# Kernel tuning notes

Hardware: AMD Instinct MI355X
Metric: run time of the kernel (lower is better)

Reference implementation:

```python
import jax, jax.numpy as jnp
import numpy as np

N, IN_CH, OUT_CH, E = 16384, 512, 512, 8


def setup_inputs() -> dict:
    key = jax.random.key(0)
    k1, k2, k3, k4 = jax.random.split(key, 4)
    x = jax.random.normal(k1, (N, IN_CH), dtype=jnp.float32)
    coefficients = jax.random.uniform(k2, (N, E), dtype=jnp.float32)
    # kaiming-uniform-ish init: bound = 1/sqrt(fan_in)
    bound = 1.0 / np.sqrt(IN_CH)
    weight = jax.random.uniform(k3, (E, OUT_CH, IN_CH), minval=-bound, maxval=bound, dtype=jnp.float32)
    bias = jax.random.uniform(k4, (E, OUT_CH), minval=-bound, maxval=bound, dtype=jnp.float32)
    return {"x": x, "coefficients": coefficients, "weight": weight, "bias": bias}


def reference(x, coefficients, weight, bias):
    # Original: mixed_weight = einsum('bc,cmn->bmn', coef, W); out = baddbmm(mixed_bias, mixed_weight, x)
    # Equivalent (by bilinearity) without materializing the (N,out,in) tensor:
    # per-expert matvec combined with coefficients in one einsum.
    out = jnp.einsum('ne,eoi,ni->no', coefficients, weight, x)
    out = out + coefficients @ bias  # (N,E) @ (E,out) -> (N,out)
    return out
```

## Files before the change

### kernel.cpp

```cpp
#include <hip/hip_runtime.h>
#include <hip/hip_bf16.h>

#define N_TOK 16384
#define CIN   512
#define COUT  512
#define NE    8
#define BM    128
#define BN    128
#define BK    64
#define KT_PER_E (CIN / BK)
#define KTILES   (NE * KT_PER_E)

typedef __attribute__((ext_vector_type(8))) short bf16x8;
typedef __attribute__((ext_vector_type(4))) float f32x4;

__device__ __forceinline__ short f2bf(float f) {
  unsigned u = __builtin_bit_cast(unsigned, f);
  u += 0x7FFFu + ((u >> 16) & 1u);
  return (short)(u >> 16);
}

__global__ void cvt_f32_bf16(const float* __restrict__ in, short* __restrict__ out, int n8) {
  int i = blockIdx.x * blockDim.x + threadIdx.x;
  if (i >= n8) return;
  const float4* p = (const float4*)in + (size_t)i * 2;
  float4 a = p[0], b = p[1];
  bf16x8 o;
  o[0] = f2bf(a.x); o[1] = f2bf(a.y); o[2] = f2bf(a.z); o[3] = f2bf(a.w);
  o[4] = f2bf(b.x); o[5] = f2bf(b.y); o[6] = f2bf(b.z); o[7] = f2bf(b.w);
  ((bf16x8*)out)[i] = o;
}

__device__ __forceinline__ void async16(short* lds, const short* g) {
  __builtin_amdgcn_global_load_lds(
      (const __attribute__((address_space(1))) void*)g,
      (__attribute__((address_space(3))) void*)lds, 16, 0, 0);
}

__global__ __launch_bounds__(256, 2)
void moe_gemm(const short* __restrict__ xb,
              const short* __restrict__ wb,
              const float* __restrict__ coef,
              const float* __restrict__ bias,
              float* __restrict__ out) {
  __shared__ short As[2][BM * BK];
  __shared__ short Bs[2][BN * BK];
  __shared__ float cf[BM * NE];

  const int tid  = threadIdx.x;
  const int lane = tid & 63;
  const int wid  = tid >> 6;
  const int wr   = wid >> 1;
  const int wc   = wid & 1;
  const int lhi  = lane >> 4;
  const int llo  = lane & 15;

  const int bid  = blockIdx.x;
  const int ct   = bid & 3;
  const int rt   = bid >> 2;
  const int row0 = rt * BM;
  const int col0 = ct * BN;

  ((float4*)cf)[tid] = ((const float4*)(coef + row0 * NE))[tid];

  const int r_st = tid >> 3;
  const int c_st = (tid & 7) * 8;
  const short* gA     = xb + (row0 + r_st) * CIN + c_st;
  const short* gBbase = wb + (col0 + r_st) * CIN + c_st;

  const int aoff = (wr * 64 + llo) * BK + lhi * 8;
  const int boff = (wc * 64 + llo) * BK + lhi * 8;

  auto STAGE = [&](int buf, int t) {
    const int e  = t >> 3;
    const int i0 = (t & 7) * BK;
    const short* ga = gA + i0;
    const short* gb = gBbase + e * (CIN * COUT) + i0;
    short* la = &As[buf][tid * 8];
    short* lb = &Bs[buf][tid * 8];
#pragma unroll
    for (int p = 0; p < 4; ++p) {
      async16(la + p * 2048, ga + p * 32 * CIN);
      async16(lb + p * 2048, gb + p * 32 * CIN);
    }
  };

  f32x4 accO[4][4];
#pragma unroll
  for (int m = 0; m < 4; ++m)
#pragma unroll
    for (int n = 0; n < 4; ++n)
      accO[m][n] = (f32x4){0.f, 0.f, 0.f, 0.f};

  STAGE(0, 0);
  __syncthreads();

  int cur = 0, t = 0;
  for (int e = 0; e < NE; ++e) {
    f32x4 accE[4][4];
#pragma unroll
    for (int m = 0; m < 4; ++m)
#pragma unroll
      for (int n = 0; n < 4; ++n)
        accE[m][n] = (f32x4){0.f, 0.f, 0.f, 0.f};

    for (int kt = 0; kt < KT_PER_E; ++kt, ++t) {
      if (t + 1 < KTILES) STAGE(cur ^ 1, t + 1);
      const short* Ab = As[cur];
      const short* Bb = Bs[cur];
#pragma unroll
      for (int ks = 0; ks < 2; ++ks) {
        bf16x8 af[4], bfr[4];
#pragma unroll
        for (int m = 0; m < 4; ++m)
          af[m] = *(const bf16x8*)&Ab[aoff + m * (16 * BK) + ks * 32];
#pragma unroll
        for (int n = 0; n < 4; ++n)
          bfr[n] = *(const bf16x8*)&Bb[boff + n * (16 * BK) + ks * 32];
#pragma unroll
        for (int m = 0; m < 4; ++m)
#pragma unroll
          for (int n = 0; n < 4; ++n)
            accE[m][n] = __builtin_amdgcn_mfma_f32_16x16x32_bf16(af[m], bfr[n], accE[m][n], 0, 0, 0);
      }
      __syncthreads();
      cur ^= 1;
    }

#pragma unroll
    for (int m = 0; m < 4; ++m)
#pragma unroll
      for (int r = 0; r < 4; ++r) {
        float c = cf[(wr * 64 + m * 16 + lhi * 4 + r) * NE + e];
#pragma unroll
        for (int n = 0; n < 4; ++n)
          accO[m][n][r] += c * accE[m][n][r];
      }
  }

  float bv[4][NE];
#pragma unroll
  for (int n = 0; n < 4; ++n) {
    int cg = col0 + wc * 64 + n * 16 + llo;
#pragma unroll
    for (int e = 0; e < NE; ++e) bv[n][e] = bias[e * COUT + cg];
  }
#pragma unroll
  for (int m = 0; m < 4; ++m)
#pragma unroll
    for (int r = 0; r < 4; ++r) {
      int row_l = wr * 64 + m * 16 + lhi * 4 + r;
      const float* cp = &cf[row_l * NE];
      float c0 = cp[0], c1 = cp[1], c2 = cp[2], c3 = cp[3],
            c4 = cp[4], c5 = cp[5], c6 = cp[6], c7 = cp[7];
      float* orow = out + (size_t)(row0 + row_l) * COUT;
#pragma unroll
      for (int n = 0; n < 4; ++n) {
        int cg = col0 + wc * 64 + n * 16 + llo;
        float bm = c0 * bv[n][0] + c1 * bv[n][1] + c2 * bv[n][2] + c3 * bv[n][3]
                 + c4 * bv[n][4] + c5 * bv[n][5] + c6 * bv[n][6] + c7 * bv[n][7];
        orow[cg] = accO[m][n][r] + bm;
      }
    }
}

extern "C" void kernel_launch(void* const* d_in, const int* in_sizes, int n_in,
                              void* d_out, int out_size, void* d_ws, size_t ws_size,
                              hipStream_t stream) {
  const float* x    = (const float*)d_in[0];
  const float* coef = (const float*)d_in[1];
  const float* w    = (const float*)d_in[2];
  const float* bias = (const float*)d_in[3];
  float* out = (float*)d_out;

  short* xb = (short*)d_ws;
  short* wb = xb + (size_t)N_TOK * CIN;

  cvt_f32_bf16<<<(N_TOK * CIN / 8) / 256, 256, 0, stream>>>(x, xb, N_TOK * CIN / 8);
  cvt_f32_bf16<<<(NE * COUT * CIN / 8) / 256, 256, 0, stream>>>(w, wb, NE * COUT * CIN / 8);

  moe_gemm<<<(N_TOK / BM) * (COUT / BN), 256, 0, stream>>>(xb, wb, coef, bias, out);
}
```

Baseline: 203.1 us.

## Rework MoE GEMM with 256-row tiles, triple buffering, swizzled LDS and fused conversion

The GEMM kernel moves to 512 threads with 256x128 output tiles (8 waves in a 2x4 layout), triple-buffered LDS with an XOR swizzle against bank conflicts, and prefetch issued two tiles ahead and interleaved with MFMA phases under s_setprio. Per-expert accumulators are folded into the output every 8 k-tiles inside a single flat loop. The two fp32-to-bf16 conversion launches become one kernel. The aim is more reuse per tile, better latency hiding, fewer launches and fewer LDS conflicts, at the cost of more LDS per block, more barriers and higher register pressure.

```diff
diff --git a/kernel.cpp b/kernel.cpp
--- a/kernel.cpp
+++ b/kernel.cpp
@@ -1,17 +1,16 @@
 #include <hip/hip_runtime.h>
-#include <hip/hip_bf16.h>
 
 #define N_TOK 16384
 #define CIN   512
 #define COUT  512
 #define NE    8
-#define BM    128
+#define BM    256
 #define BN    128
 #define BK    64
-#define KT_PER_E (CIN / BK)
-#define KTILES   (NE * KT_PER_E)
+#define KTILES   64
 
 typedef __attribute__((ext_vector_type(8))) short bf16x8;
+typedef __attribute__((ext_vector_type(4))) short s16x4;
 typedef __attribute__((ext_vector_type(4))) float f32x4;
 
 __device__ __forceinline__ short f2bf(float f) {
@@ -20,15 +19,16 @@
   return (short)(u >> 16);
 }
 
-__global__ void cvt_f32_bf16(const float* __restrict__ in, short* __restrict__ out, int n8) {
+__global__ void cvt_all(const float4* __restrict__ x, const float4* __restrict__ w,
+                        s16x4* __restrict__ xb, s16x4* __restrict__ wb) {
   int i = blockIdx.x * blockDim.x + threadIdx.x;
-  if (i >= n8) return;
-  const float4* p = (const float4*)in + (size_t)i * 2;
-  float4 a = p[0], b = p[1];
-  bf16x8 o;
-  o[0] = f2bf(a.x); o[1] = f2bf(a.y); o[2] = f2bf(a.z); o[3] = f2bf(a.w);
-  o[4] = f2bf(b.x); o[5] = f2bf(b.y); o[6] = f2bf(b.z); o[7] = f2bf(b.w);
-  ((bf16x8*)out)[i] = o;
+  const int NX = N_TOK * CIN / 4;
+  float4 v; s16x4* o;
+  if (i < NX) { v = x[i]; o = xb + i; }
+  else       { int j = i - NX; v = w[j]; o = wb + j; }
+  s16x4 r;
+  r[0] = f2bf(v.x); r[1] = f2bf(v.y); r[2] = f2bf(v.z); r[3] = f2bf(v.w);
+  *o = r;
 }
 
 __device__ __forceinline__ void async16(short* lds, const short* g) {
@@ -37,21 +37,21 @@
       (__attribute__((address_space(3))) void*)lds, 16, 0, 0);
 }
 
-__global__ __launch_bounds__(256, 2)
+__global__ __launch_bounds__(512, 2)
 void moe_gemm(const short* __restrict__ xb,
               const short* __restrict__ wb,
               const float* __restrict__ coef,
               const float* __restrict__ bias,
               float* __restrict__ out) {
-  __shared__ short As[2][BM * BK];
-  __shared__ short Bs[2][BN * BK];
+  __shared__ short As[3][BM * BK];
+  __shared__ short Bs[3][BN * BK];
   __shared__ float cf[BM * NE];
 
   const int tid  = threadIdx.x;
   const int lane = tid & 63;
   const int wid  = tid >> 6;
-  const int wr   = wid >> 1;
-  const int wc   = wid & 1;
+  const int wm   = wid >> 2;
+  const int wn   = wid & 3;
   const int lhi  = lane >> 4;
   const int llo  = lane & 15;
 
@@ -64,102 +64,133 @@
   ((float4*)cf)[tid] = ((const float4*)(coef + row0 * NE))[tid];
 
   const int r_st = tid >> 3;
-  const int c_st = (tid & 7) * 8;
-  const short* gA     = xb + (row0 + r_st) * CIN + c_st;
-  const short* gBbase = wb + (col0 + r_st) * CIN + c_st;
-
-  const int aoff = (wr * 64 + llo) * BK + lhi * 8;
-  const int boff = (wc * 64 + llo) * BK + lhi * 8;
-
-  auto STAGE = [&](int buf, int t) {
+  const int c_sw = ((tid & 7) * 8) ^ ((r_st & 7) << 3);
+  const short* gA = xb + (row0 + r_st) * CIN + c_sw;
+  const short* gB = wb + (col0 + r_st) * CIN + c_sw;
+
+  auto stageA = [&](int buf, int t, int p) {
+    const int i0 = (t & 7) * BK;
+    async16(&As[buf][p * 4096 + tid * 8], gA + p * 64 * CIN + i0);
+  };
+  auto stageB = [&](int buf, int t, int p) {
     const int e  = t >> 3;
     const int i0 = (t & 7) * BK;
-    const short* ga = gA + i0;
-    const short* gb = gBbase + e * (CIN * COUT) + i0;
-    short* la = &As[buf][tid * 8];
-    short* lb = &Bs[buf][tid * 8];
+    async16(&Bs[buf][p * 4096 + tid * 8], gB + e * (CIN * COUT) + p * 64 * CIN + i0);
+  };
+
+  const int swz0 = (lhi * 8) ^ ((llo & 7) << 3);
+  const int swz1 = (32 + lhi * 8) ^ ((llo & 7) << 3);
+  const int arow = wm * 128 + llo;
+  const int brow = wn * 32 + llo;
+
+  f32x4 accO[8][2], accE[8][2];
+#pragma unroll
+  for (int m = 0; m < 8; ++m)
+#pragma unroll
+    for (int n = 0; n < 2; ++n) {
+      accO[m][n] = (f32x4){0.f, 0.f, 0.f, 0.f};
+      accE[m][n] = (f32x4){0.f, 0.f, 0.f, 0.f};
+    }
+
+#pragma unroll
+  for (int p = 0; p < 4; ++p) stageA(0, 0, p);
+#pragma unroll
+  for (int p = 0; p < 2; ++p) stageB(0, 0, p);
+#pragma unroll
+  for (int p = 0; p < 4; ++p) stageA(1, 1, p);
+#pragma unroll
+  for (int p = 0; p < 2; ++p) stageB(1, 1, p);
+  asm volatile("s_waitcnt vmcnt(6) lgkmcnt(0)");
+  __builtin_amdgcn_s_barrier();
+
+  bf16x8 bfr[2][2];
+
+  for (int t = 0; t < KTILES; ++t) {
+    const int cur = t % 3;
+    const int nx  = (t + 2) % 3;
+    const bool pf = (t + 2) < KTILES;
+    const short* Ab = As[cur];
+    const short* Bb = Bs[cur];
+
 #pragma unroll
     for (int p = 0; p < 4; ++p) {
-      async16(la + p * 2048, ga + p * 32 * CIN);
-      async16(lb + p * 2048, gb + p * 32 * CIN);
-    }
-  };
-
-  f32x4 accO[4][4];
-#pragma unroll
-  for (int m = 0; m < 4; ++m)
-#pragma unroll
-    for (int n = 0; n < 4; ++n)
-      accO[m][n] = (f32x4){0.f, 0.f, 0.f, 0.f};
-
-  STAGE(0, 0);
-  __syncthreads();
-
-  int cur = 0, t = 0;
-  for (int e = 0; e < NE; ++e) {
-    f32x4 accE[4][4];
-#pragma unroll
-    for (int m = 0; m < 4; ++m)
-#pragma unroll
-      for (int n = 0; n < 4; ++n)
-        accE[m][n] = (f32x4){0.f, 0.f, 0.f, 0.f};
-
-    for (int kt = 0; kt < KT_PER_E; ++kt, ++t) {
-      if (t + 1 < KTILES) STAGE(cur ^ 1, t + 1);
-      const short* Ab = As[cur];
-      const short* Bb = Bs[cur];
-#pragma unroll
-      for (int ks = 0; ks < 2; ++ks) {
-        bf16x8 af[4], bfr[4];
-#pragma unroll
-        for (int m = 0; m < 4; ++m)
-          af[m] = *(const bf16x8*)&Ab[aoff + m * (16 * BK) + ks * 32];
-#pragma unroll
-        for (int n = 0; n < 4; ++n)
-          bfr[n] = *(const bf16x8*)&Bb[boff + n * (16 * BK) + ks * 32];
-#pragma unroll
-        for (int m = 0; m < 4; ++m)
-#pragma unroll
-          for (int n = 0; n < 4; ++n)
-            accE[m][n] = __builtin_amdgcn_mfma_f32_16x16x32_bf16(af[m], bfr[n], accE[m][n], 0, 0, 0);
+      bf16x8 af[2][2];
+      af[0][0] = *(const bf16x8*)&Ab[(arow + (2 * p) * 16) * 64 + swz0];
+      af[0][1] = *(const bf16x8*)&Ab[(arow + (2 * p) * 16) * 64 + swz1];
+      af[1][0] = *(const bf16x8*)&Ab[(arow + (2 * p + 1) * 16) * 64 + swz0];
+      af[1][1] = *(const bf16x8*)&Ab[(arow + (2 * p + 1) * 16) * 64 + swz1];
+      if (p == 0) {
+        bfr[0][0] = *(const bf16x8*)&Bb[(brow + 0) * 64 + swz0];
+        bfr[0][1] = *(const bf16x8*)&Bb[(brow + 0) * 64 + swz1];
+        bfr[1][0] = *(const bf16x8*)&Bb[(brow + 16) * 64 + swz0];
+        bfr[1][1] = *(const bf16x8*)&Bb[(brow + 16) * 64 + swz1];
       }
-      __syncthreads();
-      cur ^= 1;
-    }
-
-#pragma unroll
-    for (int m = 0; m < 4; ++m)
-#pragma unroll
-      for (int r = 0; r < 4; ++r) {
-        float c = cf[(wr * 64 + m * 16 + lhi * 4 + r) * NE + e];
-#pragma unroll
-        for (int n = 0; n < 4; ++n)
-          accO[m][n][r] += c * accE[m][n][r];
+      if (pf) {
+        if (p == 0)      { stageA(nx, t + 2, 0); stageA(nx, t + 2, 1); }
+        else if (p == 1) { stageA(nx, t + 2, 2); stageA(nx, t + 2, 3); }
+        else if (p == 2) { stageB(nx, t + 2, 0); stageB(nx, t + 2, 1); }
       }
+      __builtin_amdgcn_s_barrier();
+      asm volatile("s_waitcnt lgkmcnt(0)");
+      __builtin_amdgcn_s_setprio(1);
+#pragma unroll
+      for (int mm = 0; mm < 2; ++mm)
+#pragma unroll
+        for (int n = 0; n < 2; ++n)
+#pragma unroll
+          for (int ks = 0; ks < 2; ++ks)
+            accE[2 * p + mm][n] = __builtin_amdgcn_mfma_f32_16x16x32_bf16(
+                af[mm][ks], bfr[n][ks], accE[2 * p + mm][n], 0, 0, 0);
+      __builtin_amdgcn_s_setprio(0);
+      __builtin_amdgcn_s_barrier();
+    }
+
+    if ((t & 7) == 7) {
+      const int e = t >> 3;
+#pragma unroll
+      for (int m = 0; m < 8; ++m)
+#pragma unroll
+        for (int r = 0; r < 4; ++r) {
+          float c = cf[(wm * 128 + m * 16 + lhi * 4 + r) * NE + e];
+#pragma unroll
+          for (int n = 0; n < 2; ++n) {
+            accO[m][n][r] += c * accE[m][n][r];
+            accE[m][n][r] = 0.f;
+          }
+        }
+    }
+
+    if (t < KTILES - 2) {
+      asm volatile("s_waitcnt vmcnt(6)");
+      __builtin_amdgcn_s_barrier();
+    } else if (t == KTILES - 2) {
+      asm volatile("s_waitcnt vmcnt(0)");
+      __builtin_amdgcn_s_barrier();
+    }
   }
 
-  float bv[4][NE];
-#pragma unroll
-  for (int n = 0; n < 4; ++n) {
-    int cg = col0 + wc * 64 + n * 16 + llo;
-#pragma unroll
-    for (int e = 0; e < NE; ++e) bv[n][e] = bias[e * COUT + cg];
+  float bcol[2][NE];
+#pragma unroll
+  for (int n = 0; n < 2; ++n) {
+    const int cg = col0 + wn * 32 + n * 16 + llo;
+#pragma unroll
+    for (int e = 0; e < NE; ++e) bcol[n][e] = bias[e * COUT + cg];
   }
 #pragma unroll
-  for (int m = 0; m < 4; ++m)
+  for (int m = 0; m < 8; ++m)
 #pragma unroll
     for (int r = 0; r < 4; ++r) {
-      int row_l = wr * 64 + m * 16 + lhi * 4 + r;
-      const float* cp = &cf[row_l * NE];
-      float c0 = cp[0], c1 = cp[1], c2 = cp[2], c3 = cp[3],
-            c4 = cp[4], c5 = cp[5], c6 = cp[6], c7 = cp[7];
-      float* orow = out + (size_t)(row0 + row_l) * COUT;
-#pragma unroll
-      for (int n = 0; n < 4; ++n) {
-        int cg = col0 + wc * 64 + n * 16 + llo;
-        float bm = c0 * bv[n][0] + c1 * bv[n][1] + c2 * bv[n][2] + c3 * bv[n][3]
-                 + c4 * bv[n][4] + c5 * bv[n][5] + c6 * bv[n][6] + c7 * bv[n][7];
-        orow[cg] = accO[m][n][r] + bm;
+      const int rl = wm * 128 + m * 16 + lhi * 4 + r;
+      float cv[NE];
+#pragma unroll
+      for (int e = 0; e < NE; ++e) cv[e] = cf[rl * NE + e];
+      float* orow = out + (size_t)(row0 + rl) * COUT;
+#pragma unroll
+      for (int n = 0; n < 2; ++n) {
+        float bm = 0.f;
+#pragma unroll
+        for (int e = 0; e < NE; ++e) bm += cv[e] * bcol[n][e];
+        orow[col0 + wn * 32 + n * 16 + llo] = accO[m][n][r] + bm;
       }
     }
 }
@@ -176,8 +207,9 @@
   short* xb = (short*)d_ws;
   short* wb = xb + (size_t)N_TOK * CIN;
 
-  cvt_f32_bf16<<<(N_TOK * CIN / 8) / 256, 256, 0, stream>>>(x, xb, N_TOK * CIN / 8);
-  cvt_f32_bf16<<<(NE * COUT * CIN / 8) / 256, 256, 0, stream>>>(w, wb, NE * COUT * CIN / 8);
-
-  moe_gemm<<<(N_TOK / BM) * (COUT / BN), 256, 0, stream>>>(xb, wb, coef, bias, out);
-}
+  const int NX = N_TOK * CIN / 4, NW = NE * COUT * CIN / 4;
+  cvt_all<<<(NX + NW) / 256, 256, 0, stream>>>(
+      (const float4*)x, (const float4*)w, (s16x4*)xb, (s16x4*)wb);
+
+  moe_gemm<<<(N_TOK / BM) * (COUT / BN), 512, 0, stream>>>(xb, wb, coef, bias, out);
+}
```

After: 192.5 us. 1.06x faster.
